# Kernel optimization log

Hardware: AMD Instinct MI355X
Metric: run time of the kernel (lower is better)

## Reference

```python
import jax, jax.numpy as jnp
import numpy as np

N = 4096  # flattened_input_shape


def setup_inputs() -> dict:
    key = jax.random.key(0)
    ks = jax.random.split(key, 5)
    eps = 0.1
    center = jax.random.normal(ks[0], (1, N), dtype=jnp.float32)
    lb0 = center - eps  # initial interval lower bounds [1, N]
    ub0 = center + eps  # initial interval upper bounds [1, N]
    W1 = jax.random.normal(ks[1], (N, N), dtype=jnp.float32) / np.float32(np.sqrt(N))
    b1 = jax.random.normal(ks[2], (1, N), dtype=jnp.float32)
    W2 = jax.random.normal(ks[3], (N, N), dtype=jnp.float32) / np.float32(np.sqrt(N))
    b2 = jax.random.normal(ks[4], (1, N), dtype=jnp.float32)
    raw_alpha = jnp.ones((N,), dtype=jnp.float32)  # nn.Parameter init
    return {"raw_alpha": raw_alpha, "lb0": lb0, "ub0": ub0,
            "W1": W1, "b1": b1, "W2": W2, "b2": b2}


def _pos(x):
    return jnp.where(x > 0, x, jnp.zeros_like(x))


def _neg(x):
    return jnp.where(x < 0, x, jnp.zeros_like(x))


def _forward(raw_alpha, lb0, ub0, W1, b1, W2, b2):
    # ---- previous.backsubstitution(): compose affine2 over affine1 ----
    clslope, clintercept = W2, b2
    cuslope, cuintercept = W2, b2
    clp, cln = _pos(clslope), _neg(clslope)
    cup, cun = _pos(cuslope), _neg(cuslope)
    clintercept = b1 @ clp.T + b1 @ cln.T + clintercept  # [1, N]
    cuintercept = b1 @ cup.T + b1 @ cun.T + cuintercept  # [1, N]
    clslope = clp @ W1 + cln @ W1  # [N, N]
    cuslope = cup @ W1 + cun @ W1  # [N, N]
    # ---- certifier against initial interval bounds ----
    lbounds = lb0 @ _pos(clslope).T + ub0 @ _neg(clslope).T + clintercept  # [1, N]
    ubounds = ub0 @ _pos(cuslope).T + lb0 @ _neg(cuslope).T + cuintercept  # [1, N]
    # ---- DeepPolyReLU transformer ----
    alpha = jax.nn.sigmoid(raw_alpha)  # [N]
    lb = lbounds.reshape(-1)
    ub = ubounds.reshape(-1)
    denom = ub - lb
    # ub/(ub-lb) with NaN (0/0) replaced by 0, grad-safe
    relu_slope = jnp.where(denom == 0, 0.0, ub / jnp.where(denom == 0, 1.0, denom))  # [N]
    relu_intercept = (1.0 - relu_slope)[None, :] * ubounds  # [1, N]
    below = ub <= 0
    above = lb >= 0
    crossing = ~(below | above)
    base = jnp.where(above, 1.0, 0.0)  # [N]
    uslope = jnp.where(crossing, relu_slope, base)
    uintercept = jnp.where(crossing[None, :], relu_intercept, jnp.zeros((1, N), dtype=ubounds.dtype))
    lslope_v1 = jnp.where(crossing, 0.0, base)
    lslope_v2 = jnp.where(crossing, 1.0, base)
    lslope = alpha * lslope_v1 + (1.0 - alpha) * lslope_v2  # [N]
    lintercept = jnp.zeros((1, N), dtype=lbounds.dtype)
    return jnp.diag(lslope), lintercept, jnp.diag(uslope), uintercept


def reference(raw_alpha, lb0, ub0, W1, b1, W2, b2):
    return _forward(raw_alpha, lb0, ub0, W1, b1, W2, b2)
```

## Files before the change

### kernel.cpp

```cpp
#include <hip/hip_runtime.h>
#include <stdint.h>

#define N 4096

#define TILE_BYTES 524288
#define KT_BYTES   16384

#define QSCALE 256.0f
#define INV_QQ (1.0f / 65536.0f)

typedef int v8i __attribute__((ext_vector_type(8)));
typedef float f32x16 __attribute__((ext_vector_type(16)));
typedef unsigned int u32x4 __attribute__((ext_vector_type(4)));
typedef float f32x4 __attribute__((ext_vector_type(4)));

union V8 { v8i v; u32x4 h[2]; };

__device__ __forceinline__ void gload16(const unsigned char* g, unsigned char* l) {
  __builtin_amdgcn_global_load_lds(
      (const __attribute__((address_space(1))) unsigned int*)g,
      (__attribute__((address_space(3))) unsigned int*)l, 16, 0, 0);
}

__device__ __forceinline__ int pack4_fp8(float a, float b, float c, float d) {
  int r = __builtin_amdgcn_cvt_pk_fp8_f32(a, b, 0, false);
  r = __builtin_amdgcn_cvt_pk_fp8_f32(c, d, r, true);
  return r;
}

__global__ __launch_bounds__(256) void prep_w1(const float* __restrict__ W1,
                                               const float* __restrict__ lb0,
                                               const float* __restrict__ ub0,
                                               unsigned char* __restrict__ W1T,
                                               float* __restrict__ tvec) {
  __shared__ float tile[64 * 65];
  __shared__ float tdot[64];
  const int t = threadIdx.x;
  const int j0 = blockIdx.x * 64, k0 = blockIdx.y * 64;
#pragma unroll
  for (int s = 0; s < 4; ++s) {
    int ck = s * 256 + t;
    int row = ck >> 4;
    int col = (ck & 15) * 4;
    float4 v = *(const float4*)(W1 + (size_t)(k0 + row) * N + j0 + col);
    float4 l = *(const float4*)(lb0 + j0 + col);
    float4 u = *(const float4*)(ub0 + j0 + col);
    float part = v.x * 0.5f * (l.x + u.x) + v.y * 0.5f * (l.y + u.y)
               + v.z * 0.5f * (l.z + u.z) + v.w * 0.5f * (l.w + u.w);
    part += __shfl_xor(part, 1, 64);
    part += __shfl_xor(part, 2, 64);
    part += __shfl_xor(part, 4, 64);
    part += __shfl_xor(part, 8, 64);
    if ((t & 15) == 0) tdot[row] = part;
    float* d = &tile[row * 65 + col];
    d[0] = v.x; d[1] = v.y; d[2] = v.z; d[3] = v.w;
  }
  __syncthreads();
  if (t < 64) atomicAdd(&tvec[k0 + t], tdot[t]);
  int jl = t >> 2, ch = (t & 3) * 16;
  float f[16];
#pragma unroll
  for (int m = 0; m < 16; ++m) f[m] = tile[(ch + m) * 65 + jl] * QSCALE;
  uint4 o;
  o.x = (unsigned)pack4_fp8(f[0], f[1], f[2], f[3]);
  o.y = (unsigned)pack4_fp8(f[4], f[5], f[6], f[7]);
  o.z = (unsigned)pack4_fp8(f[8], f[9], f[10], f[11]);
  o.w = (unsigned)pack4_fp8(f[12], f[13], f[14], f[15]);
  int j = j0 + jl;
  int kb = k0 + ch;
  *(uint4*)(W1T + (size_t)(j >> 7) * TILE_BYTES + (size_t)(kb >> 7) * KT_BYTES
            + (size_t)((kb >> 4) & 7) * 2048 + (j & 127) * 16) = o;
}

__global__ __launch_bounds__(256) void convert_w2(const float* __restrict__ W2,
                                                  const float* __restrict__ b1,
                                                  const float* __restrict__ tvec,
                                                  unsigned char* __restrict__ W2q,
                                                  float* __restrict__ cvec,
                                                  float* __restrict__ Sc) {
  __shared__ int lpack[128][33];
  const int t = threadIdx.x;
  const int i0 = blockIdx.y * 128;
  const int k0 = blockIdx.x * 128;
  const int kl = (t & 31) * 4;
  const int rsub = t >> 5;
  float4 bv = *(const float4*)(b1 + k0 + kl);
  float4 tv = *(const float4*)(tvec + k0 + kl);
#pragma unroll
  for (int s = 0; s < 16; ++s) {
    int row = s * 8 + rsub;
    float4 w = *(const float4*)(W2 + (size_t)(i0 + row) * N + k0 + kl);
    float db = w.x * bv.x + w.y * bv.y + w.z * bv.z + w.w * bv.w;
    float dt = w.x * tv.x + w.y * tv.y + w.z * tv.z + w.w * tv.w;
    db += __shfl_xor(db, 1, 64);  dt += __shfl_xor(dt, 1, 64);
    db += __shfl_xor(db, 2, 64);  dt += __shfl_xor(dt, 2, 64);
    db += __shfl_xor(db, 4, 64);  dt += __shfl_xor(dt, 4, 64);
    db += __shfl_xor(db, 8, 64);  dt += __shfl_xor(dt, 8, 64);
    db += __shfl_xor(db, 16, 64); dt += __shfl_xor(dt, 16, 64);
    if ((t & 31) == 0) {
      atomicAdd(&cvec[i0 + row], db);
      atomicAdd(&Sc[i0 + row], dt);
    }
    lpack[row][t & 31] = pack4_fp8(w.x * QSCALE, w.y * QSCALE,
                                   w.z * QSCALE, w.w * QSCALE);
  }
  __syncthreads();
  unsigned char* panel = W2q + (size_t)blockIdx.y * TILE_BYTES
                       + (size_t)blockIdx.x * KT_BYTES;
#pragma unroll
  for (int q = 0; q < 4; ++q) {
    int cid = q * 256 + t;
    int r = cid & 127, c = cid >> 7;
    uint4 o;
    o.x = (unsigned)lpack[r][4 * c + 0];
    o.y = (unsigned)lpack[r][4 * c + 1];
    o.z = (unsigned)lpack[r][4 * c + 2];
    o.w = (unsigned)lpack[r][4 * c + 3];
    *(uint4*)(panel + (size_t)c * 2048 + r * 16) = o;
  }
}

#define NT 32
#define DSR(dst, addr, OFF) \
  asm volatile("ds_read_b128 %0, %1 offset:" OFF : "=v"(dst) : "v"(addr))

__global__ __launch_bounds__(512, 2) void gemm_absrow(const unsigned char* __restrict__ A,
                                                      const unsigned char* __restrict__ B,
                                                      const float* __restrict__ lb0,
                                                      const float* __restrict__ ub0,
                                                      float* __restrict__ R_acc) {
  __shared__ __align__(16) unsigned char sm[4 * 32768];
  const int t = threadIdx.x;
  const int lane = t & 63, w = t >> 6;
  const int wr = w >> 2, wc = w & 3;
  const int l31 = lane & 31, half = lane >> 5;

  const int bid = blockIdx.y * 16 + blockIdx.x;
  const int swz = (bid & 7) * 32 + (bid >> 3);
  const int bm = swz >> 4, bn = swz & 15;
  const int i0 = bm * 256, j0 = bn * 256;

  const unsigned char* gA0 = A + (size_t)(2 * bm) * TILE_BYTES + t * 16;
  const unsigned char* gA1 = gA0 + TILE_BYTES;
  const unsigned char* gB0 = B + (size_t)(2 * bn) * TILE_BYTES + t * 16;
  const unsigned char* gB1 = gB0 + TILE_BYTES;

  f32x16 acc[4][2] = {};
  const int sc1 = 0x7F7F7F7F;

  const unsigned lds0 =
      (unsigned)(size_t)(__attribute__((address_space(3))) unsigned char*)sm;
  const unsigned aoff = lds0 + wr * 8192 + half * 4096 + l31 * 16;
  const int jb0 = wc * 64 + l31, jb1 = jb0 + 32;
  const unsigned boff0 = lds0 + 16384 + (jb0 >> 7) * 8192 + half * 4096 + (jb0 & 127) * 16;
  const unsigned boff1 = lds0 + 16384 + (jb1 >> 7) * 8192 + half * 4096 + (jb1 & 127) * 16;

  auto stage = [&](int g) {
    unsigned char* d = sm + (size_t)(g & 3) * 32768 + t * 16;
    const size_t off = (size_t)(g >> 1) * KT_BYTES + (size_t)(g & 1) * 8192;
    gload16(gA0 + off, d);
    gload16(gA1 + off, d + 8192);
    gload16(gB0 + off, d + 16384);
    gload16(gB1 + off, d + 24576);
  };

  V8 af[4], bf[2];

#define PHASE_LOAD(g)                                                     \
  {                                                                       \
    unsigned sb = (unsigned)((g) & 3) * 32768u;                           \
    unsigned sa = aoff + sb, s0 = boff0 + sb, s1 = boff1 + sb;            \
    DSR(af[0].h[0], sa, "0");    DSR(af[0].h[1], sa, "2048");             \
    DSR(af[1].h[0], sa, "512");  DSR(af[1].h[1], sa, "2560");             \
    DSR(af[2].h[0], sa, "1024"); DSR(af[2].h[1], sa, "3072");             \
    DSR(af[3].h[0], sa, "1536"); DSR(af[3].h[1], sa, "3584");             \
    DSR(bf[0].h[0], s0, "0");    DSR(bf[0].h[1], s0, "2048");             \
    DSR(bf[1].h[0], s1, "0");    DSR(bf[1].h[1], s1, "2048");             \
  }

#define PHASE_MFMA()                                                      \
  asm volatile("s_waitcnt lgkmcnt(0)" ::: "memory");                      \
  __builtin_amdgcn_sched_barrier(0);                                      \
  __builtin_amdgcn_s_setprio(1);                                          \
  _Pragma("unroll") for (int tm = 0; tm < 4; ++tm)                        \
    _Pragma("unroll") for (int tn = 0; tn < 2; ++tn)                      \
      acc[tm][tn] = __builtin_amdgcn_mfma_scale_f32_32x32x64_f8f6f4(      \
          af[tm].v, bf[tn].v, acc[tm][tn], 0, 0, 0, sc1, 0, sc1);         \
  __builtin_amdgcn_s_setprio(0);

  stage(0); stage(1); stage(2);
  asm volatile("s_waitcnt vmcnt(8)" ::: "memory");
  __builtin_amdgcn_s_barrier();

  for (int g = 0; g < 61; ++g) {
    PHASE_LOAD(g);
    stage(g + 3);
    asm volatile("s_waitcnt vmcnt(8)" ::: "memory");
    __builtin_amdgcn_s_barrier();
    PHASE_MFMA();
    __builtin_amdgcn_s_barrier();
  }
  PHASE_LOAD(61);
  asm volatile("s_waitcnt vmcnt(4)" ::: "memory");
  __builtin_amdgcn_s_barrier();
  PHASE_MFMA();
  __builtin_amdgcn_s_barrier();
  PHASE_LOAD(62);
  asm volatile("s_waitcnt vmcnt(0)" ::: "memory");
  __builtin_amdgcn_s_barrier();
  PHASE_MFMA();
  __builtin_amdgcn_s_barrier();
  PHASE_LOAD(63);
  PHASE_MFMA();

  float epsv[2];
#pragma unroll
  for (int tn = 0; tn < 2; ++tn) {
    int j = j0 + wc * 64 + tn * 32 + l31;
    epsv[tn] = 0.5f * (ub0[j] - lb0[j]);
  }
#pragma unroll
  for (int tm = 0; tm < 4; ++tm) {
#pragma unroll
    for (int r = 0; r < 16; ++r) {
      float s = fabsf(acc[tm][0][r]) * epsv[0] + fabsf(acc[tm][1][r]) * epsv[1];
#pragma unroll
      for (int off = 1; off < 32; off <<= 1)
        s += __shfl_xor(s, off, 64);
      if (l31 == 0) {
        int i = i0 + wr * 128 + tm * 32 + (r & 3) + 8 * (r >> 2) + 4 * half;
        atomicAdd(&R_acc[i], s);
      }
    }
  }
}

struct ReluVals { float lslope, uslope, uinter; };

__device__ __forceinline__ ReluVals relu_vals(int i,
                                              const float* __restrict__ cvec,
                                              const float* __restrict__ Sc,
                                              const float* __restrict__ b2,
                                              const float* __restrict__ R_acc,
                                              const float* __restrict__ raw_alpha) {
  float mid = Sc[i] + cvec[i] + b2[i];
  float rr = R_acc[i] * INV_QQ;
  float lb = mid - rr;
  float ub = mid + rr;
  float alpha = 1.f / (1.f + expf(-raw_alpha[i]));
  float denom = ub - lb;
  float slope = (denom == 0.f) ? 0.f : ub / denom;
  bool below = ub <= 0.f, above = lb >= 0.f;
  bool crossing = !(below || above);
  float base = above ? 1.f : 0.f;
  ReluVals v;
  v.uslope = crossing ? slope : base;
  v.uinter = crossing ? (1.f - slope) * ub : 0.f;
  float l1 = crossing ? 0.f : base;
  float l2 = crossing ? 1.f : base;
  v.lslope = alpha * l1 + (1.f - alpha) * l2;
  return v;
}

__global__ __launch_bounds__(256) void fill_patch(float4* __restrict__ out, int n4,
                                                  const float* __restrict__ cvec,
                                                  const float* __restrict__ Sc,
                                                  const float* __restrict__ b2,
                                                  const float* __restrict__ R_acc,
                                                  const float* __restrict__ raw_alpha) {
  const size_t NN = (size_t)N * N;
  const size_t d1_end = NN;
  const size_t d2_beg = NN + N;
  const size_t d2_end = 2 * NN + N;
  int idx = blockIdx.x * 256 + threadIdx.x;
  int stride = gridDim.x * 256;
  for (int i = idx; i < n4; i += stride) {
    size_t e = 4 * (size_t)i;
    float4 v = make_float4(0.f, 0.f, 0.f, 0.f);
    if (e >= d2_end) {
      int b = (int)(e - d2_end);
      v.x = relu_vals(b + 0, cvec, Sc, b2, R_acc, raw_alpha).uinter;
      v.y = relu_vals(b + 1, cvec, Sc, b2, R_acc, raw_alpha).uinter;
      v.z = relu_vals(b + 2, cvec, Sc, b2, R_acc, raw_alpha).uinter;
      v.w = relu_vals(b + 3, cvec, Sc, b2, R_acc, raw_alpha).uinter;
    } else if (e < d1_end) {
      int r = (int)(e >> 12), c = (int)(e & 4095);
      if (r >= c && r < c + 4)
        (&v.x)[r - c] = relu_vals(r, cvec, Sc, b2, R_acc, raw_alpha).lslope;
    } else if (e >= d2_beg) {
      size_t e2 = e - d2_beg;
      int r = (int)(e2 >> 12), c = (int)(e2 & 4095);
      if (r >= c && r < c + 4)
        (&v.x)[r - c] = relu_vals(r, cvec, Sc, b2, R_acc, raw_alpha).uslope;
    }
    f32x4 vv = {v.x, v.y, v.z, v.w};
    __builtin_nontemporal_store(vv, (f32x4*)(out + i));
  }
}

extern "C" void kernel_launch(void* const* d_in, const int* in_sizes, int n_in,
                              void* d_out, int out_size, void* d_ws, size_t ws_size,
                              hipStream_t stream) {
  const float* raw_alpha = (const float*)d_in[0];
  const float* lb0 = (const float*)d_in[1];
  const float* ub0 = (const float*)d_in[2];
  const float* W1 = (const float*)d_in[3];
  const float* b1 = (const float*)d_in[4];
  const float* W2 = (const float*)d_in[5];
  const float* b2 = (const float*)d_in[6];

  float* tvec = (float*)d_ws;
  float* cvec = tvec + N;
  float* Sc = cvec + N;
  float* R_acc = Sc + N;

  unsigned char* W2q = (unsigned char*)d_out;
  unsigned char* W1Tq = W2q + (size_t)N * N;

  (void)hipMemsetAsync(d_ws, 0, 4 * N * sizeof(float), stream);
  prep_w1<<<dim3(N / 64, N / 64), 256, 0, stream>>>(W1, lb0, ub0, W1Tq, tvec);
  convert_w2<<<dim3(N / 128, N / 128), 256, 0, stream>>>(W2, b1, tvec, W2q, cvec, Sc);
  gemm_absrow<<<dim3(16, 16), 512, 0, stream>>>(W2q, W1Tq, lb0, ub0, R_acc);
  int n4 = out_size / 4;
  fill_patch<<<8192, 256, 0, stream>>>((float4*)d_out, n4, cvec, Sc, b2, R_acc, raw_alpha);
}
```

Before: 354.5 us.

## Single-barrier GEMM pipeline with staged LDS waits; memset output and patch diagonals

The GEMM main loop drops from two barriers per k-step to one. LDS fragment reads are reordered so the B fragments arrive first, and partial lgkmcnt waits let each MFMA pair start as soon as its A fragment is ready. The output fill kernel, which evaluated branches for every float4, is replaced by hipMemsetAsync plus a tiny kernel that writes only the diagonals and the intercept. This is meant to cut barrier stalls and the fill kernel's per-element overhead, but it relies on the single barrier still protecting 4-deep buffer reuse and on memset bandwidth.

```diff
diff --git a/kernel.cpp b/kernel.cpp
--- a/kernel.cpp
+++ b/kernel.cpp
@@ -12,7 +12,6 @@
 typedef int v8i __attribute__((ext_vector_type(8)));
 typedef float f32x16 __attribute__((ext_vector_type(16)));
 typedef unsigned int u32x4 __attribute__((ext_vector_type(4)));
-typedef float f32x4 __attribute__((ext_vector_type(4)));
 
 union V8 { v8i v; u32x4 h[2]; };
 
@@ -120,7 +119,6 @@
   }
 }
 
-#define NT 32
 #define DSR(dst, addr, OFF) \
   asm volatile("ds_read_b128 %0, %1 offset:" OFF : "=v"(dst) : "v"(addr))
 
@@ -171,44 +169,54 @@
     unsigned sb = (unsigned)((g) & 3) * 32768u;                           \
     unsigned sa = aoff + sb, s0 = boff0 + sb, s1 = boff1 + sb;            \
     DSR(af[0].h[0], sa, "0");    DSR(af[0].h[1], sa, "2048");             \
+    DSR(bf[0].h[0], s0, "0");    DSR(bf[0].h[1], s0, "2048");             \
+    DSR(bf[1].h[0], s1, "0");    DSR(bf[1].h[1], s1, "2048");             \
     DSR(af[1].h[0], sa, "512");  DSR(af[1].h[1], sa, "2560");             \
     DSR(af[2].h[0], sa, "1024"); DSR(af[2].h[1], sa, "3072");             \
     DSR(af[3].h[0], sa, "1536"); DSR(af[3].h[1], sa, "3584");             \
-    DSR(bf[0].h[0], s0, "0");    DSR(bf[0].h[1], s0, "2048");             \
-    DSR(bf[1].h[0], s1, "0");    DSR(bf[1].h[1], s1, "2048");             \
-  }
+  }
+
+#define MFMA2(tm)                                                         \
+  acc[tm][0] = __builtin_amdgcn_mfma_scale_f32_32x32x64_f8f6f4(           \
+      af[tm].v, bf[0].v, acc[tm][0], 0, 0, 0, sc1, 0, sc1);               \
+  acc[tm][1] = __builtin_amdgcn_mfma_scale_f32_32x32x64_f8f6f4(           \
+      af[tm].v, bf[1].v, acc[tm][1], 0, 0, 0, sc1, 0, sc1);
 
 #define PHASE_MFMA()                                                      \
+  __builtin_amdgcn_s_setprio(1);                                          \
+  asm volatile("s_waitcnt lgkmcnt(6)" ::: "memory");                      \
+  __builtin_amdgcn_sched_barrier(0);                                      \
+  MFMA2(0)                                                                \
+  asm volatile("s_waitcnt lgkmcnt(4)" ::: "memory");                      \
+  __builtin_amdgcn_sched_barrier(0);                                      \
+  MFMA2(1)                                                                \
+  asm volatile("s_waitcnt lgkmcnt(2)" ::: "memory");                      \
+  __builtin_amdgcn_sched_barrier(0);                                      \
+  MFMA2(2)                                                                \
   asm volatile("s_waitcnt lgkmcnt(0)" ::: "memory");                      \
   __builtin_amdgcn_sched_barrier(0);                                      \
-  __builtin_amdgcn_s_setprio(1);                                          \
-  _Pragma("unroll") for (int tm = 0; tm < 4; ++tm)                        \
-    _Pragma("unroll") for (int tn = 0; tn < 2; ++tn)                      \
-      acc[tm][tn] = __builtin_amdgcn_mfma_scale_f32_32x32x64_f8f6f4(      \
-          af[tm].v, bf[tn].v, acc[tm][tn], 0, 0, 0, sc1, 0, sc1);         \
+  MFMA2(3)                                                                \
   __builtin_amdgcn_s_setprio(0);
 
   stage(0); stage(1); stage(2);
+
+#pragma unroll 1
+  for (int g = 0; g < 61; ++g) {
+    asm volatile("s_waitcnt vmcnt(8)" ::: "memory");
+    __builtin_amdgcn_s_barrier();
+    PHASE_LOAD(g);
+    stage(g + 3);
+    PHASE_MFMA();
+  }
   asm volatile("s_waitcnt vmcnt(8)" ::: "memory");
   __builtin_amdgcn_s_barrier();
-
-  for (int g = 0; g < 61; ++g) {
-    PHASE_LOAD(g);
-    stage(g + 3);
-    asm volatile("s_waitcnt vmcnt(8)" ::: "memory");
-    __builtin_amdgcn_s_barrier();
-    PHASE_MFMA();
-    __builtin_amdgcn_s_barrier();
-  }
   PHASE_LOAD(61);
+  PHASE_MFMA();
   asm volatile("s_waitcnt vmcnt(4)" ::: "memory");
   __builtin_amdgcn_s_barrier();
+  PHASE_LOAD(62);
   PHASE_MFMA();
-  __builtin_amdgcn_s_barrier();
-  PHASE_LOAD(62);
   asm volatile("s_waitcnt vmcnt(0)" ::: "memory");
-  __builtin_amdgcn_s_barrier();
-  PHASE_MFMA();
   __builtin_amdgcn_s_barrier();
   PHASE_LOAD(63);
   PHASE_MFMA();
@@ -262,40 +270,18 @@
   return v;
 }
 
-__global__ __launch_bounds__(256) void fill_patch(float4* __restrict__ out, int n4,
+__global__ __launch_bounds__(256) void patch_diag(float* __restrict__ out,
                                                   const float* __restrict__ cvec,
                                                   const float* __restrict__ Sc,
                                                   const float* __restrict__ b2,
                                                   const float* __restrict__ R_acc,
                                                   const float* __restrict__ raw_alpha) {
   const size_t NN = (size_t)N * N;
-  const size_t d1_end = NN;
-  const size_t d2_beg = NN + N;
-  const size_t d2_end = 2 * NN + N;
-  int idx = blockIdx.x * 256 + threadIdx.x;
-  int stride = gridDim.x * 256;
-  for (int i = idx; i < n4; i += stride) {
-    size_t e = 4 * (size_t)i;
-    float4 v = make_float4(0.f, 0.f, 0.f, 0.f);
-    if (e >= d2_end) {
-      int b = (int)(e - d2_end);
-      v.x = relu_vals(b + 0, cvec, Sc, b2, R_acc, raw_alpha).uinter;
-      v.y = relu_vals(b + 1, cvec, Sc, b2, R_acc, raw_alpha).uinter;
-      v.z = relu_vals(b + 2, cvec, Sc, b2, R_acc, raw_alpha).uinter;
-      v.w = relu_vals(b + 3, cvec, Sc, b2, R_acc, raw_alpha).uinter;
-    } else if (e < d1_end) {
-      int r = (int)(e >> 12), c = (int)(e & 4095);
-      if (r >= c && r < c + 4)
-        (&v.x)[r - c] = relu_vals(r, cvec, Sc, b2, R_acc, raw_alpha).lslope;
-    } else if (e >= d2_beg) {
-      size_t e2 = e - d2_beg;
-      int r = (int)(e2 >> 12), c = (int)(e2 & 4095);
-      if (r >= c && r < c + 4)
-        (&v.x)[r - c] = relu_vals(r, cvec, Sc, b2, R_acc, raw_alpha).uslope;
-    }
-    f32x4 vv = {v.x, v.y, v.z, v.w};
-    __builtin_nontemporal_store(vv, (f32x4*)(out + i));
-  }
+  int i = blockIdx.x * 256 + threadIdx.x;
+  ReluVals v = relu_vals(i, cvec, Sc, b2, R_acc, raw_alpha);
+  out[(size_t)i * (N + 1)] = v.lslope;
+  out[NN + N + (size_t)i * (N + 1)] = v.uslope;
+  out[2 * NN + N + i] = v.uinter;
 }
 
 extern "C" void kernel_launch(void* const* d_in, const int* in_sizes, int n_in,
@@ -321,6 +307,6 @@
   prep_w1<<<dim3(N / 64, N / 64), 256, 0, stream>>>(W1, lb0, ub0, W1Tq, tvec);
   convert_w2<<<dim3(N / 128, N / 128), 256, 0, stream>>>(W2, b1, tvec, W2q, cvec, Sc);
   gemm_absrow<<<dim3(16, 16), 512, 0, stream>>>(W2q, W1Tq, lb0, ub0, R_acc);
-  int n4 = out_size / 4;
-  fill_patch<<<8192, 256, 0, stream>>>((float4*)d_out, n4, cvec, Sc, b2, R_acc, raw_alpha);
-}
+  (void)hipMemsetAsync(d_out, 0, (size_t)out_size * sizeof(float), stream);
+  patch_diag<<<N / 256, 256, 0, stream>>>((float*)d_out, cvec, Sc, b2, R_acc, raw_alpha);
+}
```

Measured after the change: 338.0 us. -4.6%, faster.
